# Kernel optimization log

Hardware: AMD Instinct MI355X
Metric: run time of the kernel (lower is better)

## Reference

```python
import jax, jax.numpy as jnp
import numpy as np

IN_DIM, OUT_DIM = 4096, 11008
NUM_SUBDIM, KS = 1376, 256
DS = OUT_DIM // NUM_SUBDIM  # 8
BATCH = 32


def setup_inputs() -> dict:
    key = jax.random.key(0)
    k1, k2, k3, k4 = jax.random.split(key, 4)
    x = jax.random.normal(k1, (BATCH, IN_DIM), dtype=jnp.float32)
    vectors = jax.random.normal(k2, (NUM_SUBDIM, KS, DS), dtype=jnp.float32)
    bias = jax.random.normal(k3, (OUT_DIM,), dtype=jnp.float32)
    indexes = jax.random.randint(k4, (IN_DIM, NUM_SUBDIM), 0, KS, dtype=jnp.int64)
    return {"x": x, "vectors": vectors, "bias": bias, "indexes": indexes}


def reference(x, vectors, bias, indexes):
    in_dim, num_subdim = indexes.shape
    ds = vectors.shape[-1]
    # PQ dequant: gather codewords per (row, subspace) -> [in_dim, num_subdim, Ds]
    # vectors[d, indexes[i, d]] via broadcast of arange(num_subdim) against indexes.
    dims = jnp.arange(num_subdim)
    weight = vectors[dims, indexes].reshape(in_dim, num_subdim * ds)  # [in_dim, out_dim]
    return x @ weight + bias
```

## Files before the change

### kernel.cpp

```cpp
#include <hip/hip_runtime.h>

#define IN_DIM  4096
#define OUT_DIM 11008
#define NSUB    1376
#define KSQ     256
#define DSUB    8
#define BATCH   32

#define DTILE   8
#define NTILE   64
#define KC      64
#define KSPLIT  16
#define KPB     (IN_DIM / KSPLIT)
#define NCHUNK  (KPB / KC)
#define NBLK    (OUT_DIM / NTILE)
#define NBLKP   176
#define NPX     (NBLKP / 8)
#define GRID_MAIN (NBLKP * KSPLIT)

typedef unsigned short ushort_t;
typedef unsigned int   uint_t;
typedef unsigned char  uchar_t;
typedef __attribute__((ext_vector_type(8))) short bf16x8;
typedef __attribute__((ext_vector_type(4))) float f32x4;

#define VEC_N    (NSUB * KSQ * DSUB)
#define XBF_OFF  (VEC_N * 2)
#define IDXT_OFF (XBF_OFF + BATCH * IN_DIM * 2)
#define SLAB_OFF (IDXT_OFF + NSUB * IN_DIM)
#define PREP_V   (VEC_N / 2)
#define PREP_X   (BATCH * IN_DIM / 2)
#define PREP_N   (PREP_V + PREP_X)
#define PACK_BLK (PREP_N / 256)
#define IDXT_BLK ((IN_DIM / 128) * (NSUB / 32))

__device__ __forceinline__ ushort_t f2bf(float f) {
    union { float f; uint_t u; } a; a.f = f;
    uint_t u = a.u;
    u += 0x7fffu + ((u >> 16) & 1u);
    return (ushort_t)(u >> 16);
}

__device__ __forceinline__ void pin4(uint4& x) {
    asm volatile("" : "+v"(x.x), "+v"(x.y), "+v"(x.z), "+v"(x.w));
}
__device__ __forceinline__ void pin1(uint_t& x) { asm volatile("" : "+v"(x)); }
__device__ __forceinline__ bf16x8 as_bf16x8(uint4 u) {
    union { uint4 u; bf16x8 v; } c; c.u = u; return c.v;
}

__global__ __launch_bounds__(256) void pq_prep(
    const float* __restrict__ x, const float* __restrict__ vecs,
    const int* __restrict__ idx,
    uint_t* __restrict__ vbf, uint_t* __restrict__ xbf,
    uchar_t* __restrict__ idx8T)
{
    __shared__ uchar_t sT[32][144];
    const int t = threadIdx.x;

    if (blockIdx.x < PACK_BLK) {
        int tid = blockIdx.x * 256 + t;
        if (tid < PREP_V) {
            float2 v = ((const float2*)vecs)[tid];
            vbf[tid] = (uint_t)f2bf(v.x) | ((uint_t)f2bf(v.y) << 16);
        } else {
            int i = tid - PREP_V;
            float2 v = ((const float2*)x)[i];
            xbf[i] = (uint_t)f2bf(v.x) | ((uint_t)f2bf(v.y) << 16);
        }
        return;
    }

    const int bid = blockIdx.x - PACK_BLK;
    const int k0 = (bid & 31) * 128, d0 = (bid >> 5) * 32;
    #pragma unroll
    for (int p = 0; p < 16; ++p) {
        int f = p * 256 + t;
        int kk = f >> 5, dd = f & 31;
        sT[dd][kk] = (uchar_t)idx[(size_t)(k0 + kk) * NSUB + d0 + dd];
    }
    __syncthreads();
    int dd = t >> 3, seg = t & 7;
    uint4 v = *(const uint4*)&sT[dd][seg * 16];
    *(uint4*)&idx8T[(size_t)(d0 + dd) * IN_DIM + k0 + seg * 16] = v;
}

__global__ __launch_bounds__(256, 4) void pq_main(
    const ushort_t* __restrict__ xbfu, const uint4* __restrict__ vbf4,
    const uchar_t* __restrict__ idx8T, float* __restrict__ slab)
{
    __shared__ uint4  sV4[4 * 512];
    __shared__ uint_t sW32[4 * 16 * 32];

    const int id  = blockIdx.x;
    const int xcd = id & 7;
    const int s   = id >> 3;
    const int nblk = xcd * NPX + (s % NPX);
    const int kblk = s / NPX;
    if (nblk >= NBLK) return;

    const int t    = threadIdx.x;
    const int w    = t >> 6;
    const int lane = t & 63;
    const int d0   = nblk * DTILE;
    const int kbase = kblk * KPB;

    const int l15 = lane & 15;
    const int l4  = lane >> 4;
    const int dl  = lane >> 5;
    const int q   = lane & 31;

    uint4 vst[8];
    {
        const size_t src0 = (size_t)(d0 + w * 2) * KSQ;
        #pragma unroll
        for (int p = 0; p < 8; ++p)
            vst[p] = vbf4[src0 + p * 64 + lane];
    }

    uint4 A[2][8];
    #pragma unroll
    for (int mt = 0; mt < 2; ++mt)
        #pragma unroll
        for (int kk = 0; kk < 8; ++kk)
            A[mt][kk] = *(const uint4*)
                &xbfu[(size_t)(mt * 16 + l15) * IN_DIM + kbase + kk * 32 + l4 * 8];

    const uchar_t* idxrow = idx8T + (size_t)(d0 + w * 2 + dl) * IN_DIM + kbase;
    uint_t bb[NCHUNK];
    #pragma unroll
    for (int c = 0; c < NCHUNK; ++c)
        bb[c] = *(const ushort_t*)&idxrow[c * KC + q * 2];

    #pragma unroll
    for (int p = 0; p < 8; ++p)
        sV4[w * 512 + p * 64 + lane] = vst[p];

    #pragma unroll
    for (int mt = 0; mt < 2; ++mt)
        #pragma unroll
        for (int kk = 0; kk < 8; ++kk)
            pin4(A[mt][kk]);
    #pragma unroll
    for (int c = 0; c < NCHUNK; ++c)
        pin1(bb[c]);

    __builtin_amdgcn_sched_barrier(0);

    f32x4 acc[2];
    acc[0] = (f32x4)0.0f; acc[1] = (f32x4)0.0f;

    const int vbase = w * 512 + dl * 256;
    const int Rbase = (w * 16 + dl * 8) * 32;

    uint4 g0 = sV4[vbase + (bb[0] & 255)];
    uint4 g1 = sV4[vbase + (bb[0] >> 8)];

    #pragma unroll
    for (int c = 0; c < NCHUNK; ++c) {
        #pragma unroll
        for (int j = 0; j < 8; ++j) {
            const uint_t sel = (j & 1) ? 0x07060302u : 0x05040100u;
            uint_t a0 = (j >> 1) == 0 ? g0.x : (j >> 1) == 1 ? g0.y : (j >> 1) == 2 ? g0.z : g0.w;
            uint_t a1 = (j >> 1) == 0 ? g1.x : (j >> 1) == 1 ? g1.y : (j >> 1) == 2 ? g1.z : g1.w;
            uint_t wv = __builtin_amdgcn_perm(a1, a0, sel);
            int dw = ((((q >> 2) ^ j) << 2) | (q & 3));
            sW32[Rbase + j * 32 + dw] = wv;
        }

        uint4 n0 = g0, n1 = g1;
        if (c + 1 < NCHUNK) {
            n0 = sV4[vbase + (bb[c + 1] & 255)];
            n1 = sV4[vbase + (bb[c + 1] >> 8)];
        }

        #pragma unroll
        for (int kq = 0; kq < 2; ++kq) {
            int u16 = (kq * 4 + l4) ^ (l15 & 7);
            bf16x8 B = *(const bf16x8*)
                ((const char*)sW32 + (w * 16 + l15) * 128 + u16 * 16);
            #pragma unroll
            for (int mt = 0; mt < 2; ++mt)
                acc[mt] = __builtin_amdgcn_mfma_f32_16x16x32_bf16(
                    as_bf16x8(A[mt][c * 2 + kq]), B, acc[mt], 0, 0, 0);
        }
        g0 = n0; g1 = n1;
    }

    float* sl = slab + (size_t)kblk * BATCH * OUT_DIM;
    const int col = nblk * NTILE + w * 16 + l15;
    #pragma unroll
    for (int mt = 0; mt < 2; ++mt)
        #pragma unroll
        for (int r = 0; r < 4; ++r)
            sl[(size_t)(mt * 16 + l4 * 4 + r) * OUT_DIM + col] = acc[mt][r];
}

__global__ __launch_bounds__(256) void pq_reduce(
    const float* __restrict__ slab, const float* __restrict__ bias,
    float* __restrict__ out)
{
    int i = blockIdx.x * 256 + threadIdx.x;
    int m = i / (OUT_DIM / 4), n4 = i - m * (OUT_DIM / 4);
    float4 s = ((const float4*)bias)[n4];
    #pragma unroll
    for (int kb = 0; kb < KSPLIT; ++kb) {
        float4 v = ((const float4*)slab)[(size_t)(kb * BATCH + m) * (OUT_DIM / 4) + n4];
        s.x += v.x; s.y += v.y; s.z += v.z; s.w += v.w;
    }
    ((float4*)out)[(size_t)m * (OUT_DIM / 4) + n4] = s;
}

extern "C" void kernel_launch(void* const* d_in, const int* in_sizes, int n_in,
                              void* d_out, int out_size, void* d_ws, size_t ws_size,
                              hipStream_t stream) {
    const float* x    = (const float*)d_in[0];
    const float* vecs = (const float*)d_in[1];
    const float* bias = (const float*)d_in[2];
    const int*   idx  = (const int*)d_in[3];
    float* out = (float*)d_out;

    uint_t*  vbf   = (uint_t*)d_ws;
    uint_t*  xbf   = (uint_t*)((char*)d_ws + XBF_OFF);
    uchar_t* idx8T = (uchar_t*)((char*)d_ws + IDXT_OFF);
    float*   slab  = (float*)((char*)d_ws + SLAB_OFF);

    pq_prep<<<PACK_BLK + IDXT_BLK, 256, 0, stream>>>(x, vecs, idx, vbf, xbf, idx8T);
    pq_main<<<GRID_MAIN, 256, 0, stream>>>(
        (const ushort_t*)xbf, (const uint4*)vbf, idx8T, slab);
    pq_reduce<<<(BATCH * OUT_DIM / 4) / 256, 256, 0, stream>>>(slab, bias, out);
}
```

Measured before the change: 114.3 us.

## Cut split-K from 16 to 4 slices, looping over four K tiles per block

Each main-kernel block now walks four 256-wide K tiles and reuses its staged codebook in LDS across them, instead of handling a single K slice. The grid shrinks from 2816 to 704 blocks, and the reduce kernel sums 4 partial slabs instead of 16. This removes repeated codebook staging and most of the slab write and read traffic. In exchange the grid is smaller, which leaves less parallelism to fill the GPU. The reloads of the x fragments between tiles are also serialized, adding some latency.

After: 111.7 us. 2.3% less time.

```diff
diff --git a/kernel.cpp b/kernel.cpp
--- a/kernel.cpp
+++ b/kernel.cpp
@@ -10,13 +10,12 @@
 #define DTILE   8
 #define NTILE   64
 #define KC      64
-#define KSPLIT  16
-#define KPB     (IN_DIM / KSPLIT)
-#define NCHUNK  (KPB / KC)
+#define NTK     4
+#define KPT     256
+#define NSLICE  4
 #define NBLK    (OUT_DIM / NTILE)
-#define NBLKP   176
-#define NPX     (NBLKP / 8)
-#define GRID_MAIN (NBLKP * KSPLIT)
+#define NPX     22
+#define GRID_MAIN (8 * NPX * NTK)
 
 typedef unsigned short ushort_t;
 typedef unsigned int   uint_t;
@@ -95,15 +94,16 @@
     const int id  = blockIdx.x;
     const int xcd = id & 7;
     const int s   = id >> 3;
-    const int nblk = xcd * NPX + (s % NPX);
-    const int kblk = s / NPX;
+    const int nl  = s % NPX;
+    const int kg  = s / NPX;
+    const int nblk = xcd * NPX + nl;
     if (nblk >= NBLK) return;
 
     const int t    = threadIdx.x;
     const int w    = t >> 6;
     const int lane = t & 63;
     const int d0   = nblk * DTILE;
-    const int kbase = kblk * KPB;
+    const int kbase = kg * (NTK * KPT);
 
     const int l15 = lane & 15;
     const int l4  = lane >> 4;
@@ -118,6 +118,12 @@
             vst[p] = vbf4[src0 + p * 64 + lane];
     }
 
+    const uchar_t* idxrow = idx8T + (size_t)(d0 + w * 2 + dl) * IN_DIM + kbase;
+    uint_t bb[NTK * 4];
+    #pragma unroll
+    for (int j = 0; j < NTK * 4; ++j)
+        bb[j] = *(const ushort_t*)&idxrow[j * KC + q * 2];
+
     uint4 A[2][8];
     #pragma unroll
     for (int mt = 0; mt < 2; ++mt)
@@ -126,12 +132,6 @@
             A[mt][kk] = *(const uint4*)
                 &xbfu[(size_t)(mt * 16 + l15) * IN_DIM + kbase + kk * 32 + l4 * 8];
 
-    const uchar_t* idxrow = idx8T + (size_t)(d0 + w * 2 + dl) * IN_DIM + kbase;
-    uint_t bb[NCHUNK];
-    #pragma unroll
-    for (int c = 0; c < NCHUNK; ++c)
-        bb[c] = *(const ushort_t*)&idxrow[c * KC + q * 2];
-
     #pragma unroll
     for (int p = 0; p < 8; ++p)
         sV4[w * 512 + p * 64 + lane] = vst[p];
@@ -142,8 +142,8 @@
         for (int kk = 0; kk < 8; ++kk)
             pin4(A[mt][kk]);
     #pragma unroll
-    for (int c = 0; c < NCHUNK; ++c)
-        pin1(bb[c]);
+    for (int j = 0; j < NTK * 4; ++j)
+        pin1(bb[j]);
 
     __builtin_amdgcn_sched_barrier(0);
 
@@ -153,41 +153,54 @@
     const int vbase = w * 512 + dl * 256;
     const int Rbase = (w * 16 + dl * 8) * 32;
 
-    uint4 g0 = sV4[vbase + (bb[0] & 255)];
-    uint4 g1 = sV4[vbase + (bb[0] >> 8)];
-
-    #pragma unroll
-    for (int c = 0; c < NCHUNK; ++c) {
-        #pragma unroll
-        for (int j = 0; j < 8; ++j) {
-            const uint_t sel = (j & 1) ? 0x07060302u : 0x05040100u;
-            uint_t a0 = (j >> 1) == 0 ? g0.x : (j >> 1) == 1 ? g0.y : (j >> 1) == 2 ? g0.z : g0.w;
-            uint_t a1 = (j >> 1) == 0 ? g1.x : (j >> 1) == 1 ? g1.y : (j >> 1) == 2 ? g1.z : g1.w;
-            uint_t wv = __builtin_amdgcn_perm(a1, a0, sel);
-            int dw = ((((q >> 2) ^ j) << 2) | (q & 3));
-            sW32[Rbase + j * 32 + dw] = wv;
+    #pragma unroll
+    for (int tile = 0; tile < NTK; ++tile) {
+        uint4 g0 = sV4[vbase + (bb[tile * 4] & 255)];
+        uint4 g1 = sV4[vbase + (bb[tile * 4] >> 8)];
+
+        #pragma unroll
+        for (int c = 0; c < 4; ++c) {
+            #pragma unroll
+            for (int j = 0; j < 8; ++j) {
+                const uint_t sel = (j & 1) ? 0x07060302u : 0x05040100u;
+                uint_t a0 = (j >> 1) == 0 ? g0.x : (j >> 1) == 1 ? g0.y : (j >> 1) == 2 ? g0.z : g0.w;
+                uint_t a1 = (j >> 1) == 0 ? g1.x : (j >> 1) == 1 ? g1.y : (j >> 1) == 2 ? g1.z : g1.w;
+                uint_t wv = __builtin_amdgcn_perm(a1, a0, sel);
+                int dw = ((((q >> 2) ^ j) << 2) | (q & 3));
+                sW32[Rbase + j * 32 + dw] = wv;
+            }
+
+            uint4 n0 = g0, n1 = g1;
+            if (tile * 4 + c + 1 < NTK * 4) {
+                n0 = sV4[vbase + (bb[tile * 4 + c + 1] & 255)];
+                n1 = sV4[vbase + (bb[tile * 4 + c + 1] >> 8)];
+            }
+
+            #pragma unroll
+            for (int kq = 0; kq < 2; ++kq) {
+                int u16 = (kq * 4 + l4) ^ (l15 & 7);
+                bf16x8 B = *(const bf16x8*)
+                    ((const char*)sW32 + (w * 16 + l15) * 128 + u16 * 16);
+                #pragma unroll
+                for (int mt = 0; mt < 2; ++mt)
+                    acc[mt] = __builtin_amdgcn_mfma_f32_16x16x32_bf16(
+                        as_bf16x8(A[mt][c * 2 + kq]), B, acc[mt], 0, 0, 0);
+            }
+            g0 = n0; g1 = n1;
         }
 
-        uint4 n0 = g0, n1 = g1;
-        if (c + 1 < NCHUNK) {
-            n0 = sV4[vbase + (bb[c + 1] & 255)];
-            n1 = sV4[vbase + (bb[c + 1] >> 8)];
-        }
-
-        #pragma unroll
-        for (int kq = 0; kq < 2; ++kq) {
-            int u16 = (kq * 4 + l4) ^ (l15 & 7);
-            bf16x8 B = *(const bf16x8*)
-                ((const char*)sW32 + (w * 16 + l15) * 128 + u16 * 16);
+        if (tile + 1 < NTK) {
+            const int kt = kbase + (tile + 1) * KPT;
             #pragma unroll
             for (int mt = 0; mt < 2; ++mt)
-                acc[mt] = __builtin_amdgcn_mfma_f32_16x16x32_bf16(
-                    as_bf16x8(A[mt][c * 2 + kq]), B, acc[mt], 0, 0, 0);
+                #pragma unroll
+                for (int kk = 0; kk < 8; ++kk)
+                    A[mt][kk] = *(const uint4*)
+                        &xbfu[(size_t)(mt * 16 + l15) * IN_DIM + kt + kk * 32 + l4 * 8];
         }
-        g0 = n0; g1 = n1;
-    }
-
-    float* sl = slab + (size_t)kblk * BATCH * OUT_DIM;
+    }
+
+    float* sl = slab + (size_t)kg * BATCH * OUT_DIM;
     const int col = nblk * NTILE + w * 16 + l15;
     #pragma unroll
     for (int mt = 0; mt < 2; ++mt)
@@ -204,7 +217,7 @@
     int m = i / (OUT_DIM / 4), n4 = i - m * (OUT_DIM / 4);
     float4 s = ((const float4*)bias)[n4];
     #pragma unroll
-    for (int kb = 0; kb < KSPLIT; ++kb) {
+    for (int kb = 0; kb < NSLICE; ++kb) {
         float4 v = ((const float4*)slab)[(size_t)(kb * BATCH + m) * (OUT_DIM / 4) + n4];
         s.x += v.x; s.y += v.y; s.z += v.z; s.w += v.w;
     }
```
